# Kernel optimization log

Hardware: AMD Instinct MI355X
Metric: run time of the kernel (lower is better)

The kernel has to match this reference:

```python
import jax, jax.numpy as jnp
import numpy as np

H, KV, D, HID, Q, S = 16, 8, 128, 2048, 1024, 8192
CACHE_POS = 4096

def rotate_half(x, axis):
    x1, x2 = jnp.split(x, 2, axis)
    return jnp.concatenate((-x2, x1), axis=axis)

def setup_inputs() -> dict:
    key = jax.random.key(0)
    ks = jax.random.split(key, 12)
    hidden_states = jax.random.normal(ks[0], (1, HID, 1, Q), jnp.float32)
    # RoPE tables for the new token positions [CACHE_POS, CACHE_POS+Q)
    pos = jnp.arange(CACHE_POS, CACHE_POS + Q, dtype=jnp.float32)
    inv_freq = 1.0 / (10000.0 ** (jnp.arange(0, D, 2, dtype=jnp.float32) / D))
    ang = pos[:, None] * inv_freq[None, :]                      # (Q, D/2)
    cos = jnp.tile(jnp.cos(ang), (1, 2))[None, None]            # (1,1,Q,D)
    sin = jnp.tile(jnp.sin(ang), (1, 2))[None, None]
    cos_t = jnp.transpose(cos, (0, 1, 3, 2))                    # (1,1,D,Q)
    sin_t = jnp.transpose(sin, (0, 1, 3, 2))
    # causal mask over full cache: key slot s visible to query i iff s <= CACHE_POS + i
    k_idx = jnp.arange(S)[:, None]
    q_idx = jnp.arange(Q)[None, :]
    attention_mask = jnp.where(k_idx <= CACHE_POS + q_idx, 0.0, -1e9).astype(jnp.float32)[None, None]  # (1,1,S,Q)
    key_cache = 0.02 * jax.random.normal(ks[1], (1, KV, S, D), jnp.float32)
    value_cache = 0.02 * jax.random.normal(ks[2], (1, KV, S, D), jnp.float32)
    w = lambda k, shp: 0.02 * jax.random.normal(k, shp, jnp.float32)
    return dict(hidden_states=hidden_states, cos=cos, sin=sin, cos_t=cos_t, sin_t=sin_t,
                attention_mask=attention_mask, key_cache=key_cache, value_cache=value_cache,
                Wq=w(ks[3], (HID, HID)), bq=w(ks[4], (HID,)),
                Wk=w(ks[5], (KV * D, HID)), bk=w(ks[6], (KV * D,)),
                Wv=w(ks[7], (KV * D, HID)), bv=w(ks[8], (KV * D,)),
                Wo=w(ks[9], (HID, HID)), cache_position=CACHE_POS)

def reference(hidden_states, cos, sin, cos_t, sin_t, attention_mask,
              key_cache, value_cache, Wq, bq, Wk, bk, Wv, bv, Wo, cache_position):
    # 1x1-conv style projections on channels-first (1, C, 1, Q)
    q = jnp.einsum('oc,bcxq->boxq', Wq, hidden_states) + bq[None, :, None, None]
    k = jnp.einsum('oc,bcxq->boxq', Wk, hidden_states) + bk[None, :, None, None]
    v = jnp.einsum('oc,bcxq->boxq', Wv, hidden_states) + bv[None, :, None, None]
    q = q.reshape(1, H, D, Q)                                   # (1,H,D,Q)
    k = k.reshape(1, KV, D, Q).transpose(0, 1, 3, 2)            # (1,KV,Q,D)
    v = v.reshape(1, KV, D, Q).transpose(0, 1, 3, 2)
    # inline RoPE: q along head_dim axis (-2), k along last axis
    q = q * cos_t + rotate_half(q, -2) * sin_t
    k = k * cos + rotate_half(k, -1) * sin
    # KV-cache scatter at layer_idx=0, offset cache_position
    key_cache = jax.lax.dynamic_update_slice(key_cache, k, (0, 0, cache_position, 0))
    value_cache = jax.lax.dynamic_update_slice(value_cache, v, (0, 0, cache_position, 0))
    k_all = key_cache[0]                                        # (KV,S,D)
    v_all = value_cache[0]
    qg = q.reshape(KV, H // KV, D, Q)                           # GQA groups
    scores = jnp.einsum('ksd,kgdq->kgsq', k_all, qg) / jnp.sqrt(jnp.float32(D))
    scores = scores + attention_mask[0]                         # (1,S,Q) broadcast
    w = jax.nn.softmax(scores, axis=2)                          # softmax over cache slots
    out = jnp.einsum('kgsq,ksd->kgdq', w, v_all)                # (KV,G,D,Q)
    out = out.reshape(1, H * D, 1, Q)
    attn_output = jnp.einsum('oc,bcxq->boxq', Wo, out)
    return attn_output
```

## Files before the change

### kernel.cpp

```cpp
#include <hip/hip_runtime.h>

#define H_HEADS 16
#define KV_HEADS 8
#define DHEAD 128
#define HID 2048
#define NQ 1024
#define SCACHE 8192
#define CPOS 4096
#define SEFF 5120

typedef __attribute__((ext_vector_type(8))) __bf16 bf16x8;
typedef __attribute__((ext_vector_type(4))) float f32x4;
typedef unsigned short u16;
typedef unsigned int u32;

__device__ __forceinline__ u16 f2b(float f) {
  u32 u = __float_as_uint(f);
  u += 0x7fffu + ((u >> 16) & 1u);
  return (u16)(u >> 16);
}
__device__ __forceinline__ u16 f2b_t(float f) {
  return (u16)(__float_as_uint(f) >> 16);
}
__device__ __forceinline__ float b2f(u16 b) { return __uint_as_float(((u32)b) << 16); }
__device__ __forceinline__ u32 pk2(u16 a, u16 b) { return (u32)a | ((u32)b << 16); }
__device__ __forceinline__ uint2 f4b4(float4 v) {
  uint2 o;
  o.x = pk2(f2b(v.x), f2b(v.y));
  o.y = pk2(f2b(v.z), f2b(v.w));
  return o;
}

__device__ __forceinline__ void gld16(const u16* g, u16* l) {
  __builtin_amdgcn_global_load_lds((const __attribute__((address_space(1))) void*)g,
                                   (__attribute__((address_space(3))) void*)l, 16, 0, 0);
}

union U4 { uint4 v; u16 u[8]; };

__global__ void __launch_bounds__(256) k_conv_w(const float* __restrict__ Wq,
                                                const float* __restrict__ Wk,
                                                const float* __restrict__ Wv,
                                                u16* __restrict__ Wb) {
  int i = blockIdx.x * 256 + threadIdx.x;
  const float* src;
  int off;
  if (i < 1048576) { src = Wq; off = i; }
  else if (i < 1572864) { src = Wk; off = i - 1048576; }
  else { src = Wv; off = i - 1572864; }
  float4 v = ((const float4*)src)[off];
  *(uint2*)(Wb + (size_t)i * 4) = f4b4(v);
}

__global__ void __launch_bounds__(256) k_f32_to_bf16(const float* __restrict__ src,
                                                     u16* __restrict__ dst, int n4) {
  int i = blockIdx.x * 256 + threadIdx.x;
  if (i < n4) {
    float4 v = ((const float4*)src)[i];
    *(uint2*)(dst + (size_t)i * 4) = f4b4(v);
  }
}

__global__ void __launch_bounds__(256) k_transpose_h(const float* __restrict__ hid,
                                                     u16* __restrict__ hT) {
  __shared__ __align__(16) float ls[64 * 68];
  int t = threadIdx.x;
  int c0 = blockIdx.x * 64, q0 = blockIdx.y * 64;
#pragma unroll
  for (int it = 0; it < 4; ++it) {
    int c = it * 256 + t;
    int row = c >> 4, ch = c & 15;
    *(float4*)(ls + row * 68 + ch * 4) =
        *(const float4*)(hid + (size_t)(c0 + row) * NQ + q0 + ch * 4);
  }
  __syncthreads();
  int ql = t & 63, cch = t >> 6;
  u32 ob[8];
#pragma unroll
  for (int j = 0; j < 8; ++j)
    ob[j] = pk2(f2b(ls[(cch * 16 + 2 * j) * 68 + ql]), f2b(ls[(cch * 16 + 2 * j + 1) * 68 + ql]));
  uint4* dst = (uint4*)(hT + (size_t)(q0 + ql) * HID + c0 + cch * 16);
  dst[0] = make_uint4(ob[0], ob[1], ob[2], ob[3]);
  dst[1] = make_uint4(ob[4], ob[5], ob[6], ob[7]);
}

__global__ void __launch_bounds__(256) k_prep_vT(const float* __restrict__ vc,
                                                 u16* __restrict__ vT) {
  __shared__ __align__(16) float ls[64 * 132];
  int t = threadIdx.x;
  int s0 = blockIdx.x * 64;
  int kv = blockIdx.y;
#pragma unroll
  for (int it = 0; it < 8; ++it) {
    int c = it * 256 + t;
    int row = c >> 5, ch = c & 31;
    *(float4*)(ls + row * 132 + ch * 4) =
        *(const float4*)(vc + ((size_t)kv * SCACHE + s0 + row) * DHEAD + ch * 4);
  }
  __syncthreads();
  int d = t >> 1, sch = t & 1;
  u32 ob[16];
#pragma unroll
  for (int j = 0; j < 16; ++j)
    ob[j] = pk2(f2b(ls[(sch * 32 + 2 * j) * 132 + d]), f2b(ls[(sch * 32 + 2 * j + 1) * 132 + d]));
  uint4* dst = (uint4*)(vT + ((size_t)kv * DHEAD + d) * SEFF + s0 + sch * 32);
#pragma unroll
  for (int j = 0; j < 4; ++j)
    dst[j] = make_uint4(ob[4 * j], ob[4 * j + 1], ob[4 * j + 2], ob[4 * j + 3]);
}

__global__ void __launch_bounds__(256) k_conv_k(const float* __restrict__ kc,
                                                u16* __restrict__ kb) {
  int i = blockIdx.x * 256 + threadIdx.x;
  int kvi = i >> 17;
  int rem = i & 131071;
  float4 v = *(const float4*)(kc + (size_t)kvi * SCACHE * DHEAD + (size_t)rem * 4);
  *(uint2*)(kb + (size_t)kvi * SEFF * DHEAD + (size_t)rem * 4) = f4b4(v);
}

__global__ void __launch_bounds__(256) k_copy_vnew(const u16* __restrict__ qkv,
                                                   u16* __restrict__ vT) {
  int i = blockIdx.x * 256 + threadIdx.x;
  int row = i >> 7, ch = i & 127;
  *(uint4*)(vT + (size_t)row * SEFF + CPOS + ch * 8) =
      *(const uint4*)(qkv + (size_t)(3072 + row) * NQ + ch * 8);
}

__global__ void __launch_bounds__(256) k_rope_t(const u16* __restrict__ qkv,
                                                const float* __restrict__ cosb,
                                                const float* __restrict__ sinb,
                                                u16* __restrict__ qb,
                                                u16* __restrict__ kb) {
  __shared__ __align__(16) u16 ls[64 * 136];
  int t = threadIdx.x;
  int hh = blockIdx.x;
  int q0 = blockIdx.y * 64;
  bool isq = hh < 16;
  int rowbase = isq ? hh * DHEAD : HID + (hh - 16) * DHEAD;
#pragma unroll
  for (int it = 0; it < 4; ++it) {
    int c = it * 256 + t;
    int d = c >> 3, qc = (c & 7) * 8;
    U4 v;
    v.v = *(const uint4*)(qkv + (size_t)(rowbase + d) * NQ + q0 + qc);
#pragma unroll
    for (int e = 0; e < 8; ++e) ls[(qc + e) * 136 + d] = v.u[e];
  }
  __syncthreads();
  int ql = t & 63, hf = t >> 6;
  int q = q0 + ql;
  float scale = isq ? 0.08838834764831845f : 1.0f;
  u16* dst = isq ? (qb + ((size_t)hh * NQ + q) * DHEAD)
                 : (kb + ((size_t)(hh - 16) * SEFF + CPOS + q) * DHEAD);
#pragma unroll
  for (int g = 0; g < 4; ++g) {
    int d0 = hf * 32 + g * 8;
    U4 x, y;
    x.v = *(uint4*)(ls + ql * 136 + d0);
    y.v = *(uint4*)(ls + ql * 136 + (d0 ^ 64));
    float4 ca = *(const float4*)(cosb + (size_t)q * DHEAD + d0);
    float4 cb = *(const float4*)(cosb + (size_t)q * DHEAD + d0 + 4);
    float4 sa = *(const float4*)(sinb + (size_t)q * DHEAD + d0);
    float4 sb = *(const float4*)(sinb + (size_t)q * DHEAD + d0 + 4);
    float cs[8] = {ca.x, ca.y, ca.z, ca.w, cb.x, cb.y, cb.z, cb.w};
    float sn[8] = {sa.x, sa.y, sa.z, sa.w, sb.x, sb.y, sb.z, sb.w};
    float sgn = (d0 < 64) ? -1.0f : 1.0f;
    u32 ob[4];
#pragma unroll
    for (int e = 0; e < 4; ++e) {
      float r0 = (b2f(x.u[2 * e]) * cs[2 * e] + sgn * b2f(y.u[2 * e]) * sn[2 * e]) * scale;
      float r1 = (b2f(x.u[2 * e + 1]) * cs[2 * e + 1] + sgn * b2f(y.u[2 * e + 1]) * sn[2 * e + 1]) * scale;
      ob[e] = pk2(f2b(r0), f2b(r1));
    }
    *(uint4*)(dst + d0) = make_uint4(ob[0], ob[1], ob[2], ob[3]);
  }
}

__global__ void __launch_bounds__(256) k_gemm_qkv(
    const u16* __restrict__ Wb, const u16* __restrict__ hT, u16* __restrict__ qkv,
    const float* __restrict__ bq, const float* __restrict__ bk, const float* __restrict__ bv) {
  __shared__ __align__(16) u16 lsA[2][128 * 32];
  __shared__ __align__(16) u16 lsB[2][64 * 32];
  int t = threadIdx.x;
  int m0 = blockIdx.x * 128, n0 = blockIdx.y * 64;
  const u16* Abase = Wb + (size_t)m0 * HID;
  const u16* Bbase = hT + (size_t)n0 * HID;
  int lane = t & 63, wid = t >> 6;
  int quad = lane >> 4, l15 = lane & 15;
  int wr = wid >> 1, wc = wid & 1;
  int ra = t >> 2, ca = (t & 3) * 8;
  f32x4 acc[4][2];
#pragma unroll
  for (int i = 0; i < 4; ++i)
#pragma unroll
    for (int j = 0; j < 2; ++j) acc[i][j] = (f32x4){0.f, 0.f, 0.f, 0.f};
  gld16(Abase + (size_t)ra * HID + ca, lsA[0] + ra * 32 + ca);
  gld16(Abase + (size_t)(64 + ra) * HID + ca, lsA[0] + (64 + ra) * 32 + ca);
  gld16(Bbase + (size_t)ra * HID + ca, lsB[0] + ra * 32 + ca);
  __syncthreads();
  int cur = 0;
  for (int kt = 0; kt < HID; kt += 32) {
    int kn = kt + 32;
    if (kn < HID) {
      gld16(Abase + (size_t)ra * HID + kn + ca, lsA[cur ^ 1] + ra * 32 + ca);
      gld16(Abase + (size_t)(64 + ra) * HID + kn + ca, lsA[cur ^ 1] + (64 + ra) * 32 + ca);
      gld16(Bbase + (size_t)ra * HID + kn + ca, lsB[cur ^ 1] + ra * 32 + ca);
    }
    bf16x8 af[4], bfr[2];
#pragma unroll
    for (int i = 0; i < 4; ++i)
      af[i] = *(const bf16x8*)(lsA[cur] + (wr * 64 + i * 16 + l15) * 32 + quad * 8);
#pragma unroll
    for (int j = 0; j < 2; ++j)
      bfr[j] = *(const bf16x8*)(lsB[cur] + (wc * 32 + j * 16 + l15) * 32 + quad * 8);
#pragma unroll
    for (int i = 0; i < 4; ++i)
#pragma unroll
      for (int j = 0; j < 2; ++j)
        acc[i][j] = __builtin_amdgcn_mfma_f32_16x16x32_bf16(af[i], bfr[j], acc[i][j], 0, 0, 0);
    __syncthreads();
    cur ^= 1;
  }
#pragma unroll
  for (int i = 0; i < 4; ++i) {
#pragma unroll
    for (int r = 0; r < 4; ++r) {
      int m = m0 + wr * 64 + i * 16 + quad * 4 + r;
      float bias = (m < 2048) ? bq[m] : ((m < 3072) ? bk[m - 2048] : bv[m - 3072]);
#pragma unroll
      for (int j = 0; j < 2; ++j) {
        int n = n0 + wc * 32 + j * 16 + l15;
        qkv[(size_t)m * NQ + n] = f2b(acc[i][j][r] + bias);
      }
    }
  }
}

__global__ void __launch_bounds__(512) k_flash(const u16* __restrict__ qb,
                                               const u16* __restrict__ kb,
                                               const u16* __restrict__ vT,
                                               u16* __restrict__ po,
                                               float* __restrict__ pm,
                                               float* __restrict__ pl) {
  __shared__ __align__(16) u16 lsK[64 * 136];
  __shared__ __align__(16) u16 lsV[128 * 72];
  __shared__ __align__(16) u16 lsP[8 * 16 * 72];
  int t = threadIdx.x;
  int h = blockIdx.x, qt = blockIdx.y, z = blockIdx.z;
  int kv = h >> 1;
  int q0 = qt * 128;
  int lane = t & 63, wid = t >> 6;
  int quad = lane >> 4, l15 = lane & 15;
  int qw = q0 + wid * 16;

  union { u16 u[8]; bf16x8 v; } onesu;
#pragma unroll
  for (int e = 0; e < 8; ++e) onesu.u[e] = 0x3f80;
  bf16x8 onesf = onesu.v;

  bf16x8 qf[4];
  const u16* qrow = qb + ((size_t)h * NQ + qw + l15) * DHEAD;
#pragma unroll
  for (int kc = 0; kc < 4; ++kc) qf[kc] = *(const bf16x8*)(qrow + kc * 32 + quad * 8);
  f32x4 oacc[8];
#pragma unroll
  for (int f = 0; f < 8; ++f) oacc[f] = (f32x4){0.f, 0.f, 0.f, 0.f};
  f32x4 lacc = (f32x4){0.f, 0.f, 0.f, 0.f};
  float m_run[4];
#pragma unroll
  for (int r = 0; r < 4; ++r) m_run[r] = -1e30f;
  u16* lsPw = lsP + wid * (16 * 72);
  int Svis = CPOS + q0 + 128;
  const u16* kbase = kb + (size_t)kv * SEFF * DHEAD;
  const u16* vbase = vT + (size_t)kv * DHEAD * SEFF;

  int rK = t >> 4, cK = (t & 15) * 8;
  int rV = t >> 3, cV = (t & 7) * 8;
  uint4 pk0, pk1, pv0, pv1;
  {
    int s0 = z * 64;
    pk0 = *(const uint4*)(kbase + (size_t)(s0 + rK) * DHEAD + cK);
    pk1 = *(const uint4*)(kbase + (size_t)(s0 + 32 + rK) * DHEAD + cK);
    pv0 = *(const uint4*)(vbase + (size_t)rV * SEFF + s0 + cV);
    pv1 = *(const uint4*)(vbase + (size_t)(64 + rV) * SEFF + s0 + cV);
  }
  for (int s0 = z * 64; s0 < Svis; s0 += 256) {
    __syncthreads();
    *(uint4*)(lsK + rK * 136 + cK) = pk0;
    *(uint4*)(lsK + (32 + rK) * 136 + cK) = pk1;
    *(uint4*)(lsV + rV * 72 + cV) = pv0;
    *(uint4*)(lsV + (64 + rV) * 72 + cV) = pv1;
    __syncthreads();
    int sn = s0 + 256;
    if (sn < Svis) {
      pk0 = *(const uint4*)(kbase + (size_t)(sn + rK) * DHEAD + cK);
      pk1 = *(const uint4*)(kbase + (size_t)(sn + 32 + rK) * DHEAD + cK);
      pv0 = *(const uint4*)(vbase + (size_t)rV * SEFF + sn + cV);
      pv1 = *(const uint4*)(vbase + (size_t)(64 + rV) * SEFF + sn + cV);
    }
    f32x4 sc[4];
#pragma unroll
    for (int js = 0; js < 4; ++js) {
      sc[js] = (f32x4){0.f, 0.f, 0.f, 0.f};
#pragma unroll
      for (int kc = 0; kc < 4; ++kc) {
        bf16x8 kf = *(const bf16x8*)(lsK + (js * 16 + l15) * 136 + kc * 32 + quad * 8);
        sc[js] = __builtin_amdgcn_mfma_f32_16x16x32_bf16(qf[kc], kf, sc[js], 0, 0, 0);
      }
    }
    if (s0 + 63 > CPOS + qw) {
#pragma unroll
      for (int r = 0; r < 4; ++r) {
        int lim = CPOS + qw + quad * 4 + r - s0;
#pragma unroll
        for (int js = 0; js < 4; ++js) {
          bool valid = (js * 16 + l15) <= lim;
          sc[js][r] = valid ? sc[js][r] : -1e30f;
        }
      }
    }
    float alpha[4];
#pragma unroll
    for (int r = 0; r < 4; ++r) {
      float mx = fmaxf(fmaxf(sc[0][r], sc[1][r]), fmaxf(sc[2][r], sc[3][r]));
      mx = fmaxf(mx, __shfl_xor(mx, 1, 64));
      mx = fmaxf(mx, __shfl_xor(mx, 2, 64));
      mx = fmaxf(mx, __shfl_xor(mx, 4, 64));
      mx = fmaxf(mx, __shfl_xor(mx, 8, 64));
      float mnew = fmaxf(m_run[r], mx);
      alpha[r] = __expf(m_run[r] - mnew);
      m_run[r] = mnew;
#pragma unroll
      for (int js = 0; js < 4; ++js) {
        float p = __expf(sc[js][r] - mnew);
        lsPw[(quad * 4 + r) * 72 + js * 16 + l15] = f2b_t(p);
      }
    }
#pragma unroll
    for (int f = 0; f < 8; ++f)
#pragma unroll
      for (int r = 0; r < 4; ++r) oacc[f][r] *= alpha[r];
#pragma unroll
    for (int r = 0; r < 4; ++r) lacc[r] *= alpha[r];
    bf16x8 pf[2];
#pragma unroll
    for (int ks = 0; ks < 2; ++ks)
      pf[ks] = *(const bf16x8*)(lsPw + l15 * 72 + ks * 32 + quad * 8);
#pragma unroll
    for (int f = 0; f < 8; ++f) {
#pragma unroll
      for (int ks = 0; ks < 2; ++ks) {
        bf16x8 vf = *(const bf16x8*)(lsV + (f * 16 + l15) * 72 + ks * 32 + quad * 8);
        oacc[f] = __builtin_amdgcn_mfma_f32_16x16x32_bf16(pf[ks], vf, oacc[f], 0, 0, 0);
      }
    }
#pragma unroll
    for (int ks = 0; ks < 2; ++ks)
      lacc = __builtin_amdgcn_mfma_f32_16x16x32_bf16(pf[ks], onesf, lacc, 0, 0, 0);
  }
  int p = (h * 8 + qt) * 4 + z;
#pragma unroll
  for (int r = 0; r < 4; ++r) {
    int qloc = wid * 16 + quad * 4 + r;
    if (l15 == 0) {
      pm[(size_t)p * 128 + qloc] = m_run[r];
      pl[(size_t)p * 128 + qloc] = lacc[r];
    }
#pragma unroll
    for (int f = 0; f < 8; ++f)
      po[(size_t)p * 16384 + qloc * 128 + f * 16 + l15] = f2b(oacc[f][r]);
  }
}

__global__ void __launch_bounds__(256) k_combine(const u16* __restrict__ po,
                                                 const float* __restrict__ pm,
                                                 const float* __restrict__ pl,
                                                 u16* __restrict__ outT) {
  int t = threadIdx.x;
  int h = blockIdx.x, qt = blockIdx.y;
  int q = qt * 64 + (t >> 2);
  int dq = (t & 3) * 32;
  int pb = (h * 8 + (q >> 7)) * 4;
  int ql = q & 127;
  float m0 = pm[(size_t)(pb + 0) * 128 + ql];
  float m1 = pm[(size_t)(pb + 1) * 128 + ql];
  float m2 = pm[(size_t)(pb + 2) * 128 + ql];
  float m3 = pm[(size_t)(pb + 3) * 128 + ql];
  float M = fmaxf(fmaxf(m0, m1), fmaxf(m2, m3));
  float w[4] = {__expf(m0 - M), __expf(m1 - M), __expf(m2 - M), __expf(m3 - M)};
  float L = 0.f;
#pragma unroll
  for (int zz = 0; zz < 4; ++zz) L += w[zz] * pl[(size_t)(pb + zz) * 128 + ql];
  float acc[32];
#pragma unroll
  for (int e = 0; e < 32; ++e) acc[e] = 0.f;
#pragma unroll
  for (int zz = 0; zz < 4; ++zz) {
    const u16* src = po + (size_t)(pb + zz) * 16384 + ql * 128 + dq;
#pragma unroll
    for (int j = 0; j < 4; ++j) {
      U4 v;
      v.v = *(const uint4*)(src + j * 8);
#pragma unroll
      for (int e = 0; e < 8; ++e) acc[j * 8 + e] += w[zz] * b2f(v.u[e]);
    }
  }
  float inv = 1.0f / L;
  u16* dst = outT + (size_t)q * HID + h * DHEAD + dq;
#pragma unroll
  for (int j = 0; j < 4; ++j) {
    u32 ob[4];
#pragma unroll
    for (int e = 0; e < 4; ++e)
      ob[e] = pk2(f2b(acc[j * 8 + 2 * e] * inv), f2b(acc[j * 8 + 2 * e + 1] * inv));
    *(uint4*)(dst + j * 8) = make_uint4(ob[0], ob[1], ob[2], ob[3]);
  }
}

__global__ void __launch_bounds__(256) k_gemm_bt(const u16* __restrict__ A,
                                                 const u16* __restrict__ BT,
                                                 float* __restrict__ C) {
  __shared__ __align__(16) u16 lsA[2][64 * 32];
  __shared__ __align__(16) u16 lsB[2][64 * 32];
  int t = threadIdx.x;
  int m0 = blockIdx.x * 64, n0 = blockIdx.y * 64;
  const u16* Abase = A + (size_t)m0 * HID;
  const u16* Bbase = BT + (size_t)n0 * HID;
  int lane = t & 63, wid = t >> 6;
  int quad = lane >> 4, l15 = lane & 15;
  int wr = wid >> 1, wc = wid & 1;
  int ra = t >> 2, ca = (t & 3) * 8;
  f32x4 acc[2][2];
#pragma unroll
  for (int i = 0; i < 2; ++i)
#pragma unroll
    for (int j = 0; j < 2; ++j) acc[i][j] = (f32x4){0.f, 0.f, 0.f, 0.f};
  gld16(Abase + (size_t)ra * HID + ca, lsA[0] + ra * 32 + ca);
  gld16(Bbase + (size_t)ra * HID + ca, lsB[0] + ra * 32 + ca);
  __syncthreads();
  int cur = 0;
  for (int kt = 0; kt < HID; kt += 32) {
    int kn = kt + 32;
    if (kn < HID) {
      gld16(Abase + (size_t)ra * HID + kn + ca, lsA[cur ^ 1] + ra * 32 + ca);
      gld16(Bbase + (size_t)ra * HID + kn + ca, lsB[cur ^ 1] + ra * 32 + ca);
    }
    bf16x8 af[2], bfr[2];
#pragma unroll
    for (int i = 0; i < 2; ++i)
      af[i] = *(const bf16x8*)(lsA[cur] + (wr * 32 + i * 16 + l15) * 32 + quad * 8);
#pragma unroll
    for (int j = 0; j < 2; ++j)
      bfr[j] = *(const bf16x8*)(lsB[cur] + (wc * 32 + j * 16 + l15) * 32 + quad * 8);
#pragma unroll
    for (int i = 0; i < 2; ++i)
#pragma unroll
      for (int j = 0; j < 2; ++j)
        acc[i][j] = __builtin_amdgcn_mfma_f32_16x16x32_bf16(af[i], bfr[j], acc[i][j], 0, 0, 0);
    __syncthreads();
    cur ^= 1;
  }
#pragma unroll
  for (int i = 0; i < 2; ++i)
#pragma unroll
    for (int r = 0; r < 4; ++r) {
      int m = m0 + wr * 32 + i * 16 + quad * 4 + r;
#pragma unroll
      for (int j = 0; j < 2; ++j) {
        int n = n0 + wc * 32 + j * 16 + l15;
        C[(size_t)m * NQ + n] = acc[i][j][r];
      }
    }
}

extern "C" void kernel_launch(void* const* d_in, const int* in_sizes, int n_in,
                              void* d_out, int out_size, void* d_ws, size_t ws_size,
                              hipStream_t stream) {
  (void)in_sizes; (void)n_in; (void)out_size; (void)ws_size;
  const float* hidden = (const float*)d_in[0];
  const float* cosb = (const float*)d_in[1];
  const float* sinb = (const float*)d_in[2];
  const float* kcache = (const float*)d_in[6];
  const float* vcache = (const float*)d_in[7];
  const float* Wq = (const float*)d_in[8];
  const float* bq = (const float*)d_in[9];
  const float* Wk = (const float*)d_in[10];
  const float* bk = (const float*)d_in[11];
  const float* Wv = (const float*)d_in[12];
  const float* bv = (const float*)d_in[13];
  const float* Wo = (const float*)d_in[14];

  char* ws = (char*)d_ws;
  u16* qkv = (u16*)(ws);
  u16* outT = (u16*)(ws + 8388608);
  u16* hT = outT;
  u16* vT = (u16*)(ws + 12582912);
  u16* Wob = vT;
  u16* kb = (u16*)(ws + 23068672);
  u16* qb = (u16*)(ws + 33554432);
  u16* Wb = (u16*)(ws + 12582912);
  u16* po = (u16*)(ws + 37748736);
  float* pm = (float*)(ws + 54525952);
  float* pl = (float*)(ws + 54788096);
  float* outb = (float*)d_out;

  k_conv_w<<<8192, 256, 0, stream>>>(Wq, Wk, Wv, Wb);
  k_transpose_h<<<dim3(32, 16), 256, 0, stream>>>(hidden, hT);
  k_gemm_qkv<<<dim3(32, 16), 256, 0, stream>>>(Wb, hT, qkv, bq, bk, bv);
  k_prep_vT<<<dim3(64, 8), 256, 0, stream>>>(vcache, vT);
  k_conv_k<<<4096, 256, 0, stream>>>(kcache, kb);
  k_rope_t<<<dim3(24, 16), 256, 0, stream>>>(qkv, cosb, sinb, qb, kb);
  k_copy_vnew<<<512, 256, 0, stream>>>(qkv, vT);
  k_flash<<<dim3(16, 8, 4), 512, 0, stream>>>(qb, kb, vT, po, pm, pl);
  k_f32_to_bf16<<<4096, 256, 0, stream>>>(Wo, Wob, 1048576);
  k_combine<<<dim3(16, 16), 256, 0, stream>>>(po, pm, pl, outT);
  k_gemm_bt<<<dim3(32, 16), 256, 0, stream>>>(Wob, outT, outb);
}
```

Baseline: 349.1 us.

## Fuse weight bf16 conversion into GEMM loads and merge small prep kernels

Removes the standalone Wq/Wk/Wv and Wo fp32-to-bf16 conversion kernels. Both GEMMs now load fp32 weights into registers, convert them, and store bf16 into LDS inside the double-buffered loop. It also merges the K-cache conversion with the V transpose, and the V-new copy with the rope kernel, cutting launches. This avoids a round trip of the weights through the workspace. The cost is that A tiles go through registers instead of direct global-to-LDS loads, and fp32 reads are twice as wide for every tile reuse across N blocks. The conversion also changes from round-to-nearest to the compiler's __bf16 cast.

```diff
diff --git a/kernel.cpp b/kernel.cpp
--- a/kernel.cpp
+++ b/kernel.cpp
@@ -38,29 +38,6 @@
 
 union U4 { uint4 v; u16 u[8]; };
 
-__global__ void __launch_bounds__(256) k_conv_w(const float* __restrict__ Wq,
-                                                const float* __restrict__ Wk,
-                                                const float* __restrict__ Wv,
-                                                u16* __restrict__ Wb) {
-  int i = blockIdx.x * 256 + threadIdx.x;
-  const float* src;
-  int off;
-  if (i < 1048576) { src = Wq; off = i; }
-  else if (i < 1572864) { src = Wk; off = i - 1048576; }
-  else { src = Wv; off = i - 1572864; }
-  float4 v = ((const float4*)src)[off];
-  *(uint2*)(Wb + (size_t)i * 4) = f4b4(v);
-}
-
-__global__ void __launch_bounds__(256) k_f32_to_bf16(const float* __restrict__ src,
-                                                     u16* __restrict__ dst, int n4) {
-  int i = blockIdx.x * 256 + threadIdx.x;
-  if (i < n4) {
-    float4 v = ((const float4*)src)[i];
-    *(uint2*)(dst + (size_t)i * 4) = f4b4(v);
-  }
-}
-
 __global__ void __launch_bounds__(256) k_transpose_h(const float* __restrict__ hid,
                                                      u16* __restrict__ hT) {
   __shared__ __align__(16) float ls[64 * 68];
@@ -84,12 +61,24 @@
   dst[1] = make_uint4(ob[4], ob[5], ob[6], ob[7]);
 }
 
-__global__ void __launch_bounds__(256) k_prep_vT(const float* __restrict__ vc,
+__global__ void __launch_bounds__(256) k_prep_kv(const float* __restrict__ kc,
+                                                 const float* __restrict__ vc,
+                                                 u16* __restrict__ kb,
                                                  u16* __restrict__ vT) {
   __shared__ __align__(16) float ls[64 * 132];
   int t = threadIdx.x;
-  int s0 = blockIdx.x * 64;
-  int kv = blockIdx.y;
+  int bx = blockIdx.x;
+  if (bx < 4096) {
+    int i = bx * 256 + t;
+    int kvi = i >> 17;
+    int rem = i & 131071;
+    float4 v = *(const float4*)(kc + (size_t)kvi * SCACHE * DHEAD + (size_t)rem * 4);
+    *(uint2*)(kb + (size_t)kvi * SEFF * DHEAD + (size_t)rem * 4) = f4b4(v);
+    return;
+  }
+  int bb = bx - 4096;
+  int s0 = (bb & 63) * 64;
+  int kv = bb >> 6;
 #pragma unroll
   for (int it = 0; it < 8; ++it) {
     int c = it * 256 + t;
@@ -109,31 +98,26 @@
     dst[j] = make_uint4(ob[4 * j], ob[4 * j + 1], ob[4 * j + 2], ob[4 * j + 3]);
 }
 
-__global__ void __launch_bounds__(256) k_conv_k(const float* __restrict__ kc,
-                                                u16* __restrict__ kb) {
-  int i = blockIdx.x * 256 + threadIdx.x;
-  int kvi = i >> 17;
-  int rem = i & 131071;
-  float4 v = *(const float4*)(kc + (size_t)kvi * SCACHE * DHEAD + (size_t)rem * 4);
-  *(uint2*)(kb + (size_t)kvi * SEFF * DHEAD + (size_t)rem * 4) = f4b4(v);
-}
-
-__global__ void __launch_bounds__(256) k_copy_vnew(const u16* __restrict__ qkv,
-                                                   u16* __restrict__ vT) {
-  int i = blockIdx.x * 256 + threadIdx.x;
-  int row = i >> 7, ch = i & 127;
-  *(uint4*)(vT + (size_t)row * SEFF + CPOS + ch * 8) =
-      *(const uint4*)(qkv + (size_t)(3072 + row) * NQ + ch * 8);
-}
-
 __global__ void __launch_bounds__(256) k_rope_t(const u16* __restrict__ qkv,
                                                 const float* __restrict__ cosb,
                                                 const float* __restrict__ sinb,
                                                 u16* __restrict__ qb,
-                                                u16* __restrict__ kb) {
+                                                u16* __restrict__ kb,
+                                                u16* __restrict__ vT) {
   __shared__ __align__(16) u16 ls[64 * 136];
   int t = threadIdx.x;
   int hh = blockIdx.x;
+  if (hh >= 24) {
+    int blk = (hh - 24) * 16 + blockIdx.y;
+#pragma unroll
+    for (int it = 0; it < 16; ++it) {
+      int i = (blk * 16 + it) * 256 + t;
+      int row = i >> 7, ch = i & 127;
+      *(uint4*)(vT + (size_t)row * SEFF + CPOS + ch * 8) =
+          *(const uint4*)(qkv + (size_t)(3072 + row) * NQ + ch * 8);
+    }
+    return;
+  }
   int q0 = blockIdx.y * 64;
   bool isq = hh < 16;
   int rowbase = isq ? hh * DHEAD : HID + (hh - 16) * DHEAD;
@@ -177,34 +161,58 @@
 }
 
 __global__ void __launch_bounds__(256) k_gemm_qkv(
-    const u16* __restrict__ Wb, const u16* __restrict__ hT, u16* __restrict__ qkv,
+    const float* __restrict__ Wq, const float* __restrict__ Wk, const float* __restrict__ Wv,
+    const u16* __restrict__ hT, u16* __restrict__ qkv,
     const float* __restrict__ bq, const float* __restrict__ bk, const float* __restrict__ bv) {
   __shared__ __align__(16) u16 lsA[2][128 * 32];
   __shared__ __align__(16) u16 lsB[2][64 * 32];
   int t = threadIdx.x;
   int m0 = blockIdx.x * 128, n0 = blockIdx.y * 64;
-  const u16* Abase = Wb + (size_t)m0 * HID;
+  const float* Asrc;
+  int mrel;
+  if (blockIdx.x < 16) { Asrc = Wq; mrel = m0; }
+  else if (blockIdx.x < 24) { Asrc = Wk; mrel = m0 - 2048; }
+  else { Asrc = Wv; mrel = m0 - 3072; }
+  const float* Abase = Asrc + (size_t)mrel * HID;
   const u16* Bbase = hT + (size_t)n0 * HID;
   int lane = t & 63, wid = t >> 6;
   int quad = lane >> 4, l15 = lane & 15;
   int wr = wid >> 1, wc = wid & 1;
-  int ra = t >> 2, ca = (t & 3) * 8;
+  int rA = t >> 1, cA = (t & 1) * 16;
+  int rB = t >> 2, cB = (t & 3) * 8;
+  u16* lsAw0;
   f32x4 acc[4][2];
 #pragma unroll
   for (int i = 0; i < 4; ++i)
 #pragma unroll
     for (int j = 0; j < 2; ++j) acc[i][j] = (f32x4){0.f, 0.f, 0.f, 0.f};
-  gld16(Abase + (size_t)ra * HID + ca, lsA[0] + ra * 32 + ca);
-  gld16(Abase + (size_t)(64 + ra) * HID + ca, lsA[0] + (64 + ra) * 32 + ca);
-  gld16(Bbase + (size_t)ra * HID + ca, lsB[0] + ra * 32 + ca);
+  float4 fa0, fa1, fa2, fa3;
+  fa0 = *(const float4*)(Abase + (size_t)rA * HID + cA);
+  fa1 = *(const float4*)(Abase + (size_t)rA * HID + cA + 4);
+  fa2 = *(const float4*)(Abase + (size_t)rA * HID + cA + 8);
+  fa3 = *(const float4*)(Abase + (size_t)rA * HID + cA + 12);
+  gld16(Bbase + (size_t)rB * HID + cB, lsB[0] + rB * 32 + cB);
+  {
+    union { bf16x8 v; uint4 q; } p0, p1;
+    p0.v[0] = (__bf16)fa0.x; p0.v[1] = (__bf16)fa0.y; p0.v[2] = (__bf16)fa0.z; p0.v[3] = (__bf16)fa0.w;
+    p0.v[4] = (__bf16)fa1.x; p0.v[5] = (__bf16)fa1.y; p0.v[6] = (__bf16)fa1.z; p0.v[7] = (__bf16)fa1.w;
+    p1.v[0] = (__bf16)fa2.x; p1.v[1] = (__bf16)fa2.y; p1.v[2] = (__bf16)fa2.z; p1.v[3] = (__bf16)fa2.w;
+    p1.v[4] = (__bf16)fa3.x; p1.v[5] = (__bf16)fa3.y; p1.v[6] = (__bf16)fa3.z; p1.v[7] = (__bf16)fa3.w;
+    lsAw0 = lsA[0] + rA * 32 + cA;
+    *(uint4*)lsAw0 = p0.q;
+    *(uint4*)(lsAw0 + 8) = p1.q;
+  }
   __syncthreads();
   int cur = 0;
   for (int kt = 0; kt < HID; kt += 32) {
     int kn = kt + 32;
-    if (kn < HID) {
-      gld16(Abase + (size_t)ra * HID + kn + ca, lsA[cur ^ 1] + ra * 32 + ca);
-      gld16(Abase + (size_t)(64 + ra) * HID + kn + ca, lsA[cur ^ 1] + (64 + ra) * 32 + ca);
-      gld16(Bbase + (size_t)ra * HID + kn + ca, lsB[cur ^ 1] + ra * 32 + ca);
+    bool more = kn < HID;
+    if (more) {
+      fa0 = *(const float4*)(Abase + (size_t)rA * HID + kn + cA);
+      fa1 = *(const float4*)(Abase + (size_t)rA * HID + kn + cA + 4);
+      fa2 = *(const float4*)(Abase + (size_t)rA * HID + kn + cA + 8);
+      fa3 = *(const float4*)(Abase + (size_t)rA * HID + kn + cA + 12);
+      gld16(Bbase + (size_t)rB * HID + kn + cB, lsB[cur ^ 1] + rB * 32 + cB);
     }
     bf16x8 af[4], bfr[2];
 #pragma unroll
@@ -218,6 +226,16 @@
 #pragma unroll
       for (int j = 0; j < 2; ++j)
         acc[i][j] = __builtin_amdgcn_mfma_f32_16x16x32_bf16(af[i], bfr[j], acc[i][j], 0, 0, 0);
+    if (more) {
+      union { bf16x8 v; uint4 q; } p0, p1;
+      p0.v[0] = (__bf16)fa0.x; p0.v[1] = (__bf16)fa0.y; p0.v[2] = (__bf16)fa0.z; p0.v[3] = (__bf16)fa0.w;
+      p0.v[4] = (__bf16)fa1.x; p0.v[5] = (__bf16)fa1.y; p0.v[6] = (__bf16)fa1.z; p0.v[7] = (__bf16)fa1.w;
+      p1.v[0] = (__bf16)fa2.x; p1.v[1] = (__bf16)fa2.y; p1.v[2] = (__bf16)fa2.z; p1.v[3] = (__bf16)fa2.w;
+      p1.v[4] = (__bf16)fa3.x; p1.v[5] = (__bf16)fa3.y; p1.v[6] = (__bf16)fa3.z; p1.v[7] = (__bf16)fa3.w;
+      u16* w = lsA[cur ^ 1] + rA * 32 + cA;
+      *(uint4*)w = p0.q;
+      *(uint4*)(w + 8) = p1.q;
+    }
     __syncthreads();
     cur ^= 1;
   }
@@ -417,33 +435,44 @@
   }
 }
 
-__global__ void __launch_bounds__(256) k_gemm_bt(const u16* __restrict__ A,
+__global__ void __launch_bounds__(256) k_gemm_bt(const float* __restrict__ Wo,
                                                  const u16* __restrict__ BT,
                                                  float* __restrict__ C) {
   __shared__ __align__(16) u16 lsA[2][64 * 32];
   __shared__ __align__(16) u16 lsB[2][64 * 32];
   int t = threadIdx.x;
   int m0 = blockIdx.x * 64, n0 = blockIdx.y * 64;
-  const u16* Abase = A + (size_t)m0 * HID;
+  const float* Abase = Wo + (size_t)m0 * HID;
   const u16* Bbase = BT + (size_t)n0 * HID;
   int lane = t & 63, wid = t >> 6;
   int quad = lane >> 4, l15 = lane & 15;
   int wr = wid >> 1, wc = wid & 1;
-  int ra = t >> 2, ca = (t & 3) * 8;
+  int rA = t >> 2, cA = (t & 3) * 8;
+  int rB = t >> 2, cB = (t & 3) * 8;
   f32x4 acc[2][2];
 #pragma unroll
   for (int i = 0; i < 2; ++i)
 #pragma unroll
     for (int j = 0; j < 2; ++j) acc[i][j] = (f32x4){0.f, 0.f, 0.f, 0.f};
-  gld16(Abase + (size_t)ra * HID + ca, lsA[0] + ra * 32 + ca);
-  gld16(Bbase + (size_t)ra * HID + ca, lsB[0] + ra * 32 + ca);
+  float4 fa0, fa1;
+  fa0 = *(const float4*)(Abase + (size_t)rA * HID + cA);
+  fa1 = *(const float4*)(Abase + (size_t)rA * HID + cA + 4);
+  gld16(Bbase + (size_t)rB * HID + cB, lsB[0] + rB * 32 + cB);
+  {
+    union { bf16x8 v; uint4 q; } p;
+    p.v[0] = (__bf16)fa0.x; p.v[1] = (__bf16)fa0.y; p.v[2] = (__bf16)fa0.z; p.v[3] = (__bf16)fa0.w;
+    p.v[4] = (__bf16)fa1.x; p.v[5] = (__bf16)fa1.y; p.v[6] = (__bf16)fa1.z; p.v[7] = (__bf16)fa1.w;
+    *(uint4*)(lsA[0] + rA * 32 + cA) = p.q;
+  }
   __syncthreads();
   int cur = 0;
   for (int kt = 0; kt < HID; kt += 32) {
     int kn = kt + 32;
-    if (kn < HID) {
-      gld16(Abase + (size_t)ra * HID + kn + ca, lsA[cur ^ 1] + ra * 32 + ca);
-      gld16(Bbase + (size_t)ra * HID + kn + ca, lsB[cur ^ 1] + ra * 32 + ca);
+    bool more = kn < HID;
+    if (more) {
+      fa0 = *(const float4*)(Abase + (size_t)rA * HID + kn + cA);
+      fa1 = *(const float4*)(Abase + (size_t)rA * HID + kn + cA + 4);
+      gld16(Bbase + (size_t)rB * HID + kn + cB, lsB[cur ^ 1] + rB * 32 + cB);
     }
     bf16x8 af[2], bfr[2];
 #pragma unroll
@@ -457,6 +486,12 @@
 #pragma unroll
       for (int j = 0; j < 2; ++j)
         acc[i][j] = __builtin_amdgcn_mfma_f32_16x16x32_bf16(af[i], bfr[j], acc[i][j], 0, 0, 0);
+    if (more) {
+      union { bf16x8 v; uint4 q; } p;
+      p.v[0] = (__bf16)fa0.x; p.v[1] = (__bf16)fa0.y; p.v[2] = (__bf16)fa0.z; p.v[3] = (__bf16)fa0.w;
+      p.v[4] = (__bf16)fa1.x; p.v[5] = (__bf16)fa1.y; p.v[6] = (__bf16)fa1.z; p.v[7] = (__bf16)fa1.w;
+      *(uint4*)(lsA[cur ^ 1] + rA * 32 + cA) = p.q;
+    }
     __syncthreads();
     cur ^= 1;
   }
@@ -495,24 +530,18 @@
   u16* outT = (u16*)(ws + 8388608);
   u16* hT = outT;
   u16* vT = (u16*)(ws + 12582912);
-  u16* Wob = vT;
   u16* kb = (u16*)(ws + 23068672);
   u16* qb = (u16*)(ws + 33554432);
-  u16* Wb = (u16*)(ws + 12582912);
   u16* po = (u16*)(ws + 37748736);
   float* pm = (float*)(ws + 54525952);
   float* pl = (float*)(ws + 54788096);
   float* outb = (float*)d_out;
 
-  k_conv_w<<<8192, 256, 0, stream>>>(Wq, Wk, Wv, Wb);
   k_transpose_h<<<dim3(32, 16), 256, 0, stream>>>(hidden, hT);
-  k_gemm_qkv<<<dim3(32, 16), 256, 0, stream>>>(Wb, hT, qkv, bq, bk, bv);
-  k_prep_vT<<<dim3(64, 8), 256, 0, stream>>>(vcache, vT);
-  k_conv_k<<<4096, 256, 0, stream>>>(kcache, kb);
-  k_rope_t<<<dim3(24, 16), 256, 0, stream>>>(qkv, cosb, sinb, qb, kb);
-  k_copy_vnew<<<512, 256, 0, stream>>>(qkv, vT);
+  k_prep_kv<<<4608, 256, 0, stream>>>(kcache, vcache, kb, vT);
+  k_gemm_qkv<<<dim3(32, 16), 256, 0, stream>>>(Wq, Wk, Wv, hT, qkv, bq, bk, bv);
+  k_rope_t<<<dim3(26, 16), 256, 0, stream>>>(qkv, cosb, sinb, qb, kb, vT);
   k_flash<<<dim3(16, 8, 4), 512, 0, stream>>>(qb, kb, vT, po, pm, pl);
-  k_f32_to_bf16<<<4096, 256, 0, stream>>>(Wo, Wob, 1048576);
   k_combine<<<dim3(16, 16), 256, 0, stream>>>(po, pm, pl, outT);
-  k_gemm_bt<<<dim3(32, 16), 256, 0, stream>>>(Wob, outT, outb);
-}
+  k_gemm_bt<<<dim3(32, 16), 256, 0, stream>>>(Wo, outT, outb);
+}
```

Result: slower. 387.1 us (+10.9%).

## Merge weight and K-cache conversion kernels and deepen GEMM K-step to 64

Applied to the files above, without the earlier changes.

Fuses the QKV weight conversion and K-cache fp32-to-bf16 conversion into one launch, moving the weight buffer into the partials region so it no longer overlaps the K-cache destination. The QKV GEMM tile shrinks from 128x64 to 64x64, doubling the grid, and both GEMMs now stage 64-wide K chunks per iteration, which halves the loop trips and barriers. This cuts launch overhead and synchronization, at the cost of more LDS per block and less A-reuse in the QKV GEMM.

```diff
diff --git a/kernel.cpp b/kernel.cpp
--- a/kernel.cpp
+++ b/kernel.cpp
@@ -38,18 +38,28 @@
 
 union U4 { uint4 v; u16 u[8]; };
 
-__global__ void __launch_bounds__(256) k_conv_w(const float* __restrict__ Wq,
-                                                const float* __restrict__ Wk,
-                                                const float* __restrict__ Wv,
-                                                u16* __restrict__ Wb) {
+__global__ void __launch_bounds__(256) k_conv_all(const float* __restrict__ Wq,
+                                                  const float* __restrict__ Wk,
+                                                  const float* __restrict__ Wv,
+                                                  const float* __restrict__ kc,
+                                                  u16* __restrict__ Wb,
+                                                  u16* __restrict__ kb) {
   int i = blockIdx.x * 256 + threadIdx.x;
-  const float* src;
-  int off;
-  if (i < 1048576) { src = Wq; off = i; }
-  else if (i < 1572864) { src = Wk; off = i - 1048576; }
-  else { src = Wv; off = i - 1572864; }
-  float4 v = ((const float4*)src)[off];
-  *(uint2*)(Wb + (size_t)i * 4) = f4b4(v);
+  if (i < 2097152) {
+    const float* src;
+    int off;
+    if (i < 1048576) { src = Wq; off = i; }
+    else if (i < 1572864) { src = Wk; off = i - 1048576; }
+    else { src = Wv; off = i - 1572864; }
+    float4 v = ((const float4*)src)[off];
+    *(uint2*)(Wb + (size_t)i * 4) = f4b4(v);
+  } else {
+    int j = i - 2097152;
+    int kvi = j >> 17;
+    int rem = j & 131071;
+    float4 v = *(const float4*)(kc + (size_t)kvi * SCACHE * DHEAD + (size_t)rem * 4);
+    *(uint2*)(kb + (size_t)kvi * SEFF * DHEAD + (size_t)rem * 4) = f4b4(v);
+  }
 }
 
 __global__ void __launch_bounds__(256) k_f32_to_bf16(const float* __restrict__ src,
@@ -107,15 +117,6 @@
 #pragma unroll
   for (int j = 0; j < 4; ++j)
     dst[j] = make_uint4(ob[4 * j], ob[4 * j + 1], ob[4 * j + 2], ob[4 * j + 3]);
-}
-
-__global__ void __launch_bounds__(256) k_conv_k(const float* __restrict__ kc,
-                                                u16* __restrict__ kb) {
-  int i = blockIdx.x * 256 + threadIdx.x;
-  int kvi = i >> 17;
-  int rem = i & 131071;
-  float4 v = *(const float4*)(kc + (size_t)kvi * SCACHE * DHEAD + (size_t)rem * 4);
-  *(uint2*)(kb + (size_t)kvi * SEFF * DHEAD + (size_t)rem * 4) = f4b4(v);
 }
 
 __global__ void __launch_bounds__(256) k_copy_vnew(const u16* __restrict__ qkv,
@@ -179,53 +180,58 @@
 __global__ void __launch_bounds__(256) k_gemm_qkv(
     const u16* __restrict__ Wb, const u16* __restrict__ hT, u16* __restrict__ qkv,
     const float* __restrict__ bq, const float* __restrict__ bk, const float* __restrict__ bv) {
-  __shared__ __align__(16) u16 lsA[2][128 * 32];
-  __shared__ __align__(16) u16 lsB[2][64 * 32];
-  int t = threadIdx.x;
-  int m0 = blockIdx.x * 128, n0 = blockIdx.y * 64;
+  __shared__ __align__(16) u16 lsA[2][2][64 * 32];
+  __shared__ __align__(16) u16 lsB[2][2][64 * 32];
+  int t = threadIdx.x;
+  int m0 = blockIdx.x * 64, n0 = blockIdx.y * 64;
   const u16* Abase = Wb + (size_t)m0 * HID;
   const u16* Bbase = hT + (size_t)n0 * HID;
   int lane = t & 63, wid = t >> 6;
   int quad = lane >> 4, l15 = lane & 15;
   int wr = wid >> 1, wc = wid & 1;
-  int ra = t >> 2, ca = (t & 3) * 8;
-  f32x4 acc[4][2];
-#pragma unroll
-  for (int i = 0; i < 4; ++i)
+  int sr = t >> 2, scol = (t & 3) * 8;
+  f32x4 acc[2][2];
+#pragma unroll
+  for (int i = 0; i < 2; ++i)
 #pragma unroll
     for (int j = 0; j < 2; ++j) acc[i][j] = (f32x4){0.f, 0.f, 0.f, 0.f};
-  gld16(Abase + (size_t)ra * HID + ca, lsA[0] + ra * 32 + ca);
-  gld16(Abase + (size_t)(64 + ra) * HID + ca, lsA[0] + (64 + ra) * 32 + ca);
-  gld16(Bbase + (size_t)ra * HID + ca, lsB[0] + ra * 32 + ca);
+  gld16(Abase + (size_t)sr * HID + scol, lsA[0][0] + t * 8);
+  gld16(Abase + (size_t)sr * HID + 32 + scol, lsA[0][1] + t * 8);
+  gld16(Bbase + (size_t)sr * HID + scol, lsB[0][0] + t * 8);
+  gld16(Bbase + (size_t)sr * HID + 32 + scol, lsB[0][1] + t * 8);
   __syncthreads();
   int cur = 0;
-  for (int kt = 0; kt < HID; kt += 32) {
-    int kn = kt + 32;
+  for (int kt = 0; kt < HID; kt += 64) {
+    int kn = kt + 64;
     if (kn < HID) {
-      gld16(Abase + (size_t)ra * HID + kn + ca, lsA[cur ^ 1] + ra * 32 + ca);
-      gld16(Abase + (size_t)(64 + ra) * HID + kn + ca, lsA[cur ^ 1] + (64 + ra) * 32 + ca);
-      gld16(Bbase + (size_t)ra * HID + kn + ca, lsB[cur ^ 1] + ra * 32 + ca);
-    }
-    bf16x8 af[4], bfr[2];
-#pragma unroll
-    for (int i = 0; i < 4; ++i)
-      af[i] = *(const bf16x8*)(lsA[cur] + (wr * 64 + i * 16 + l15) * 32 + quad * 8);
-#pragma unroll
-    for (int j = 0; j < 2; ++j)
-      bfr[j] = *(const bf16x8*)(lsB[cur] + (wc * 32 + j * 16 + l15) * 32 + quad * 8);
-#pragma unroll
-    for (int i = 0; i < 4; ++i)
+      gld16(Abase + (size_t)sr * HID + kn + scol, lsA[cur ^ 1][0] + t * 8);
+      gld16(Abase + (size_t)sr * HID + kn + 32 + scol, lsA[cur ^ 1][1] + t * 8);
+      gld16(Bbase + (size_t)sr * HID + kn + scol, lsB[cur ^ 1][0] + t * 8);
+      gld16(Bbase + (size_t)sr * HID + kn + 32 + scol, lsB[cur ^ 1][1] + t * 8);
+    }
+#pragma unroll
+    for (int kk = 0; kk < 2; ++kk) {
+      bf16x8 af[2], bfr[2];
+#pragma unroll
+      for (int i = 0; i < 2; ++i)
+        af[i] = *(const bf16x8*)(lsA[cur][kk] + (wr * 32 + i * 16 + l15) * 32 + quad * 8);
 #pragma unroll
       for (int j = 0; j < 2; ++j)
-        acc[i][j] = __builtin_amdgcn_mfma_f32_16x16x32_bf16(af[i], bfr[j], acc[i][j], 0, 0, 0);
+        bfr[j] = *(const bf16x8*)(lsB[cur][kk] + (wc * 32 + j * 16 + l15) * 32 + quad * 8);
+#pragma unroll
+      for (int i = 0; i < 2; ++i)
+#pragma unroll
+        for (int j = 0; j < 2; ++j)
+          acc[i][j] = __builtin_amdgcn_mfma_f32_16x16x32_bf16(af[i], bfr[j], acc[i][j], 0, 0, 0);
+    }
     __syncthreads();
     cur ^= 1;
   }
 #pragma unroll
-  for (int i = 0; i < 4; ++i) {
+  for (int i = 0; i < 2; ++i) {
 #pragma unroll
     for (int r = 0; r < 4; ++r) {
-      int m = m0 + wr * 64 + i * 16 + quad * 4 + r;
+      int m = m0 + wr * 32 + i * 16 + quad * 4 + r;
       float bias = (m < 2048) ? bq[m] : ((m < 3072) ? bk[m - 2048] : bv[m - 3072]);
 #pragma unroll
       for (int j = 0; j < 2; ++j) {
@@ -420,8 +426,8 @@
 __global__ void __launch_bounds__(256) k_gemm_bt(const u16* __restrict__ A,
                                                  const u16* __restrict__ BT,
                                                  float* __restrict__ C) {
-  __shared__ __align__(16) u16 lsA[2][64 * 32];
-  __shared__ __align__(16) u16 lsB[2][64 * 32];
+  __shared__ __align__(16) u16 lsA[2][2][64 * 32];
+  __shared__ __align__(16) u16 lsB[2][2][64 * 32];
   int t = threadIdx.x;
   int m0 = blockIdx.x * 64, n0 = blockIdx.y * 64;
   const u16* Abase = A + (size_t)m0 * HID;
@@ -429,34 +435,41 @@
   int lane = t & 63, wid = t >> 6;
   int quad = lane >> 4, l15 = lane & 15;
   int wr = wid >> 1, wc = wid & 1;
-  int ra = t >> 2, ca = (t & 3) * 8;
+  int sr = t >> 2, scol = (t & 3) * 8;
   f32x4 acc[2][2];
 #pragma unroll
   for (int i = 0; i < 2; ++i)
 #pragma unroll
     for (int j = 0; j < 2; ++j) acc[i][j] = (f32x4){0.f, 0.f, 0.f, 0.f};
-  gld16(Abase + (size_t)ra * HID + ca, lsA[0] + ra * 32 + ca);
-  gld16(Bbase + (size_t)ra * HID + ca, lsB[0] + ra * 32 + ca);
+  gld16(Abase + (size_t)sr * HID + scol, lsA[0][0] + t * 8);
+  gld16(Abase + (size_t)sr * HID + 32 + scol, lsA[0][1] + t * 8);
+  gld16(Bbase + (size_t)sr * HID + scol, lsB[0][0] + t * 8);
+  gld16(Bbase + (size_t)sr * HID + 32 + scol, lsB[0][1] + t * 8);
   __syncthreads();
   int cur = 0;
-  for (int kt = 0; kt < HID; kt += 32) {
-    int kn = kt + 32;
+  for (int kt = 0; kt < HID; kt += 64) {
+    int kn = kt + 64;
     if (kn < HID) {
-      gld16(Abase + (size_t)ra * HID + kn + ca, lsA[cur ^ 1] + ra * 32 + ca);
-      gld16(Bbase + (size_t)ra * HID + kn + ca, lsB[cur ^ 1] + ra * 32 + ca);
-    }
-    bf16x8 af[2], bfr[2];
-#pragma unroll
-    for (int i = 0; i < 2; ++i)
-      af[i] = *(const bf16x8*)(lsA[cur] + (wr * 32 + i * 16 + l15) * 32 + quad * 8);
-#pragma unroll
-    for (int j = 0; j < 2; ++j)
-      bfr[j] = *(const bf16x8*)(lsB[cur] + (wc * 32 + j * 16 + l15) * 32 + quad * 8);
-#pragma unroll
-    for (int i = 0; i < 2; ++i)
+      gld16(Abase + (size_t)sr * HID + kn + scol, lsA[cur ^ 1][0] + t * 8);
+      gld16(Abase + (size_t)sr * HID + kn + 32 + scol, lsA[cur ^ 1][1] + t * 8);
+      gld16(Bbase + (size_t)sr * HID + kn + scol, lsB[cur ^ 1][0] + t * 8);
+      gld16(Bbase + (size_t)sr * HID + kn + 32 + scol, lsB[cur ^ 1][1] + t * 8);
+    }
+#pragma unroll
+    for (int kk = 0; kk < 2; ++kk) {
+      bf16x8 af[2], bfr[2];
+#pragma unroll
+      for (int i = 0; i < 2; ++i)
+        af[i] = *(const bf16x8*)(lsA[cur][kk] + (wr * 32 + i * 16 + l15) * 32 + quad * 8);
 #pragma unroll
       for (int j = 0; j < 2; ++j)
-        acc[i][j] = __builtin_amdgcn_mfma_f32_16x16x32_bf16(af[i], bfr[j], acc[i][j], 0, 0, 0);
+        bfr[j] = *(const bf16x8*)(lsB[cur][kk] + (wc * 32 + j * 16 + l15) * 32 + quad * 8);
+#pragma unroll
+      for (int i = 0; i < 2; ++i)
+#pragma unroll
+        for (int j = 0; j < 2; ++j)
+          acc[i][j] = __builtin_amdgcn_mfma_f32_16x16x32_bf16(af[i], bfr[j], acc[i][j], 0, 0, 0);
+    }
     __syncthreads();
     cur ^= 1;
   }
@@ -498,17 +511,16 @@
   u16* Wob = vT;
   u16* kb = (u16*)(ws + 23068672);
   u16* qb = (u16*)(ws + 33554432);
-  u16* Wb = (u16*)(ws + 12582912);
   u16* po = (u16*)(ws + 37748736);
+  u16* Wb = po;
   float* pm = (float*)(ws + 54525952);
   float* pl = (float*)(ws + 54788096);
   float* outb = (float*)d_out;
 
-  k_conv_w<<<8192, 256, 0, stream>>>(Wq, Wk, Wv, Wb);
+  k_conv_all<<<12288, 256, 0, stream>>>(Wq, Wk, Wv, kcache, Wb, kb);
   k_transpose_h<<<dim3(32, 16), 256, 0, stream>>>(hidden, hT);
-  k_gemm_qkv<<<dim3(32, 16), 256, 0, stream>>>(Wb, hT, qkv, bq, bk, bv);
+  k_gemm_qkv<<<dim3(64, 16), 256, 0, stream>>>(Wb, hT, qkv, bq, bk, bv);
   k_prep_vT<<<dim3(64, 8), 256, 0, stream>>>(vcache, vT);
-  k_conv_k<<<4096, 256, 0, stream>>>(kcache, kb);
   k_rope_t<<<dim3(24, 16), 256, 0, stream>>>(qkv, cosb, sinb, qb, kb);
   k_copy_vnew<<<512, 256, 0, stream>>>(qkv, vT);
   k_flash<<<dim3(16, 8, 4), 512, 0, stream>>>(qb, kb, vT, po, pm, pl);
```

New measurement: 340.1 us. 1.03x faster.
